# Kernel tuning notes

Measured on AMD Instinct MI355X. Metric: run time of the kernel, lower is better.

## Reference

```python
import jax, jax.numpy as jnp
import numpy as np


def setup_inputs() -> dict:
    key = jax.random.key(0)
    ks = jax.random.split(key, 10)
    B, T, V, D, H = 64, 256, 32000, 512, 1024
    s = lambda fan: 1.0 / np.sqrt(fan)
    return {
        "tokens": jax.random.randint(ks[0], (B, T), 0, V, dtype=jnp.int32),
        "emb": jax.random.normal(ks[1], (V, D), dtype=jnp.float32) * 0.05,
        "W": jax.random.normal(ks[2], (D, 4 * H), dtype=jnp.float32) * s(D),
        "U": jax.random.normal(ks[3], (H, 4 * H), dtype=jnp.float32) * s(H),
        "b": jnp.zeros((4 * H,), dtype=jnp.float32),
        "Wm": jax.random.normal(ks[4], (H, H), dtype=jnp.float32) * s(H),
        "bm": jnp.zeros((H,), dtype=jnp.float32),
        "Wv": jax.random.normal(ks[5], (H, H), dtype=jnp.float32) * s(H),
        "bv": jnp.zeros((H,), dtype=jnp.float32),
        "eps": jax.random.normal(ks[6], (B, H), dtype=jnp.float32),
    }


def _lstm_masked(x_emb, mask, W, U, b):
    # x_emb: [B,T,D], mask: [B,T] bool (True = valid token)
    B, T, D = x_emb.shape
    H = U.shape[0]
    # Precompute input projections for all timesteps: [B,T,4H]
    xW = jnp.einsum('btd,df->btf', x_emb, W) + b

    def step(carry, inp):
        h, c = carry
        xw_t, m_t = inp  # [B,4H], [B]
        z = xw_t + h @ U  # [B,4H]
        i, f, g, o = jnp.split(z, 4, axis=-1)
        i = jax.nn.sigmoid(i)
        f = jax.nn.sigmoid(f)
        g = jnp.tanh(g)
        o = jax.nn.sigmoid(o)
        c_new = f * c + i * g
        h_new = o * jnp.tanh(c_new)
        m = m_t[:, None]
        # Masked timesteps carry state through unchanged (Keras mask_zero semantics)
        h = jnp.where(m, h_new, h)
        c = jnp.where(m, c_new, c)
        return (h, c), None

    h0 = jnp.zeros((B, H), dtype=x_emb.dtype)
    c0 = jnp.zeros((B, H), dtype=x_emb.dtype)
    (h, c), _ = jax.lax.scan(step, (h0, c0),
                             (jnp.swapaxes(xW, 0, 1), jnp.swapaxes(mask, 0, 1)))
    return h


def reference(tokens, emb, W, U, b, Wm, bm, Wv, bv, eps):
    mask = tokens != 0                      # mask_zero=True
    x = emb[tokens]                          # [B,T,D] embedding lookup
    h = _lstm_masked(x, mask, W, U, b)       # [B,H] final state
    mean = h @ Wm + bm
    logvar = h @ Wv + bv
    latent = eps * jnp.exp(logvar * 0.5) + mean   # reparameterization trick
    return latent
```

## Files before the change

kernel.cpp:

```cpp
#include <hip/hip_runtime.h>
#include <stdint.h>

#define BB 64
#define TT 256
#define VV 32000
#define DD 512
#define HH 1024
#define FH 4096

#define UCOL 1040
#define ULDS (128 * UCOL)
#define LSTM_LDS (ULDS + 1024)
#define RSTRIDE (TT * FH * 2)

typedef float f32x4 __attribute__((ext_vector_type(4)));
typedef int   i32x4 __attribute__((ext_vector_type(4)));
typedef __bf16 bf16x8 __attribute__((ext_vector_type(8)));

typedef __attribute__((address_space(1))) void void_g;
typedef __attribute__((address_space(3))) void void_l;

static __device__ __forceinline__ void gload_lds16(const void* g, void* l) {
  __builtin_amdgcn_global_load_lds((const void_g*)g, (void_l*)l, 16, 0, 0);
}

static __device__ __forceinline__ unsigned short f2bf(float f) {
  union { float f; unsigned u; } x; x.f = f;
  unsigned r = x.u + 0x7FFFu + ((x.u >> 16) & 1u);
  return (unsigned short)(r >> 16);
}
static __device__ __forceinline__ float bf2f(unsigned short s) {
  union { unsigned u; float f; } x; x.u = ((unsigned)s) << 16;
  return x.f;
}
static __device__ __forceinline__ i32x4 as_i32x4(uint4 v) {
  union { uint4 u; i32x4 i; } x; x.u = v; return x.i;
}
static __device__ __forceinline__ float sigm(float x) {
  return 1.f / (1.f + __expf(-x));
}
static __device__ __forceinline__ float tanh_f(float x) {
  x = fminf(15.f, fmaxf(-15.f, x));
  float e = __expf(2.f * x);
  return (e - 1.f) / (e + 1.f);
}


__global__ void k_cast_emb(const float* __restrict__ src, unsigned short* __restrict__ dst) {
  size_t i = ((size_t)blockIdx.x * 256 + threadIdx.x) * 8;
  float4 a = *(const float4*)(src + i);
  float4 b = *(const float4*)(src + i + 4);
  uint4 o;
  o.x = (unsigned)f2bf(a.x) | ((unsigned)f2bf(a.y) << 16);
  o.y = (unsigned)f2bf(a.z) | ((unsigned)f2bf(a.w) << 16);
  o.z = (unsigned)f2bf(b.x) | ((unsigned)f2bf(b.y) << 16);
  o.w = (unsigned)f2bf(b.z) | ((unsigned)f2bf(b.w) << 16);
  *(uint4*)(dst + i) = o;
}

__global__ void k_prep_w(const float* __restrict__ Wsrc, unsigned short* __restrict__ Wt) {
  int n = blockIdx.x;
  int k0 = threadIdx.x * 4;
  unsigned short q0 = f2bf(Wsrc[(size_t)(k0 + 0) * FH + n]);
  unsigned short q1 = f2bf(Wsrc[(size_t)(k0 + 1) * FH + n]);
  unsigned short q2 = f2bf(Wsrc[(size_t)(k0 + 2) * FH + n]);
  unsigned short q3 = f2bf(Wsrc[(size_t)(k0 + 3) * FH + n]);
  uint2 o;
  o.x = (unsigned)q0 | ((unsigned)q1 << 16);
  o.y = (unsigned)q2 | ((unsigned)q3 << 16);
  *(uint2*)((char*)Wt + (size_t)n * 1024 + (size_t)k0 * 2) = o;
}

__global__ void k_prep_uq(const float* __restrict__ Usrc, char* __restrict__ Uq,
                          float* __restrict__ su) {
  __shared__ float red[4];
  int bid = blockIdx.x;
  int s = bid >> 7, c = bid & 127;
  int g = c >> 5, m = c & 31;
  int n = g * 1024 + s * 32 + m;
  int tid = threadIdx.x, lane = tid & 63, wid = tid >> 6;
  float v[4];
  float mx = 0.f;
  #pragma unroll
  for (int j = 0; j < 4; ++j) {
    v[j] = Usrc[(size_t)(tid * 4 + j) * FH + n];
    mx = fmaxf(mx, fabsf(v[j]));
  }
  #pragma unroll
  for (int off = 32; off; off >>= 1) mx = fmaxf(mx, __shfl_xor(mx, off));
  if (lane == 0) red[wid] = mx;
  __syncthreads();
  mx = fmaxf(fmaxf(red[0], red[1]), fmaxf(red[2], red[3]));
  float inv = mx > 0.f ? 127.f / mx : 0.f;
  unsigned pk = 0;
  #pragma unroll
  for (int j = 0; j < 4; ++j) {
    int q = __float2int_rn(v[j] * inv);
    pk |= ((unsigned)q & 255u) << (8 * j);
  }
  *(unsigned*)(Uq + (size_t)s * 131072 + (size_t)c * 1024 + tid * 4) = pk;
  if (tid == 0) su[s * 128 + c] = mx / 16129.f;
}

__global__ void k_mask(const int* __restrict__ tok, unsigned long long* __restrict__ mask64) {
  int t = threadIdx.x;
  unsigned long long m = 0;
  for (int b = 0; b < BB; ++b)
    m |= (unsigned long long)(tok[b * TT + t] != 0) << b;
  mask64[t] = m;
}


__launch_bounds__(256)
__global__ void k_gemm_xw(const int* __restrict__ tok, const unsigned short* __restrict__ embb,
                          const unsigned short* __restrict__ Wt, const float* __restrict__ bsrc,
                          unsigned short* __restrict__ xw) {
  __shared__ char As[16384];
  __shared__ char Bs[16384];
  __shared__ int toks[128];
  int tid = threadIdx.x, lane = tid & 63, wid = tid >> 6;
  int bm = blockIdx.x >> 5, bn = blockIdx.x & 31;
  if (tid < 128) toks[tid] = tok[bm * 128 + tid];
  int wm = wid >> 1, wn = wid & 1;
  f32x4 vz = {0.f, 0.f, 0.f, 0.f};
  f32x4 acc[4][4];
  #pragma unroll
  for (int i = 0; i < 4; ++i)
    #pragma unroll
    for (int j = 0; j < 4; ++j) acc[i][j] = vz;

  int kls = (lane >> 4) * 16;
  for (int ks = 0; ks < 8; ++ks) {
    __syncthreads();
    #pragma unroll
    for (int c = 0; c < 4; ++c) {
      int o = wid * 4096 + c * 1024 + lane * 16;
      int m = o >> 7, kl = o & 127;
      const char* ga = (const char*)embb + (size_t)toks[m] * 1024 + ks * 128 + (kl ^ ((m & 7) << 4));
      gload_lds16(ga, As + o);
      const char* gb = (const char*)Wt + (size_t)(bn * 128 + m) * 1024 + ks * 128 + (kl ^ ((m & 7) << 4));
      gload_lds16(gb, Bs + o);
    }
    asm volatile("s_waitcnt vmcnt(0)" ::: "memory");
    __syncthreads();
    #pragma unroll
    for (int tk = 0; tk < 2; ++tk) {
      bf16x8 af[4], bf[4];
      int kb = tk * 64 + kls;
      #pragma unroll
      for (int mt = 0; mt < 4; ++mt) {
        int m = wm * 64 + mt * 16 + (lane & 15);
        af[mt] = *(const bf16x8*)(As + m * 128 + (kb ^ ((m & 7) << 4)));
      }
      #pragma unroll
      for (int nt = 0; nt < 4; ++nt) {
        int n = wn * 64 + nt * 16 + (lane & 15);
        bf[nt] = *(const bf16x8*)(Bs + n * 128 + (kb ^ ((n & 7) << 4)));
      }
      #pragma unroll
      for (int mt = 0; mt < 4; ++mt)
        #pragma unroll
        for (int nt = 0; nt < 4; ++nt)
          acc[mt][nt] = __builtin_amdgcn_mfma_f32_16x16x32_bf16(af[mt], bf[nt], acc[mt][nt], 0, 0, 0);
    }
  }
  #pragma unroll
  for (int nt = 0; nt < 4; ++nt) {
    int n = bn * 128 + wn * 64 + nt * 16 + (lane & 15);
    float bias = bsrc[n];
    int g = n >> 10, hid = n & 1023, s = hid >> 5, m = hid & 31;
    int p = s * 128 + m * 4 + g;
    #pragma unroll
    for (int mt = 0; mt < 4; ++mt) {
      #pragma unroll
      for (int r = 0; r < 4; ++r) {
        int row = bm * 128 + wm * 64 + mt * 16 + (lane >> 4) * 4 + r;
        xw[(size_t)row * FH + p] = f2bf(acc[mt][nt][r] + bias);
      }
    }
  }
}


#define GATE(R) do { \
  unsigned long long x_ = xg[R]; \
  float zi_ = (float)aI[R] * s0 + bf2f((unsigned short)(x_ & 0xFFFFu)); \
  float zf_ = (float)aF[R] * s1 + bf2f((unsigned short)((x_ >> 16) & 0xFFFFu)); \
  float zg_ = (float)aG[R] * s2 + bf2f((unsigned short)((x_ >> 32) & 0xFFFFu)); \
  float zo_ = (float)aO[R] * s3 + bf2f((unsigned short)((x_ >> 48) & 0xFFFFu)); \
  float I_ = sigm(zi_), F_ = sigm(zf_), G_ = tanh_f(zg_), O_ = sigm(zo_); \
  float cn_ = F_ * cst[R] + I_ * G_; \
  float hn_ = O_ * tanh_f(cn_); \
  if (!((mb >> (grp * 16 + lq * 4 + (R))) & 1ull)) { cn_ = cst[R]; hn_ = hst[R]; } \
  cst[R] = cn_; hst[R] = hn_; \
  hs[hh * 320 + (lq * 4 + (R)) * 20 + l15] = (char)__float2int_rn(hn_ * 127.f); \
  if (t == TT - 1) hfin[(size_t)(grp * 16 + lq * 4 + (R)) * 1024 + rank * 32 + hh * 16 + l15] = hn_; \
} while (0)

__launch_bounds__(128, 1)
__global__ void k_lstm(const char* __restrict__ Uq, const float* __restrict__ su,
                       const unsigned short* __restrict__ xw,
                       const unsigned long long* __restrict__ mask64,
                       char* __restrict__ hseq, unsigned* __restrict__ flags,
                       float* __restrict__ hfin) {
  extern __shared__ char smem[];
  char* Us = smem;
  char* hs = smem + ULDS;
  int tid = threadIdx.x, lane = tid & 63, hh = tid >> 6;
  int l15 = lane & 15, lq = lane >> 4;
  int grp = blockIdx.x >> 5, rank = blockIdx.x & 31;
  int m = hh * 16 + l15;

  {
    const char* src = Uq + (size_t)rank * 131072;
    #pragma unroll 4
    for (int i = 0; i < 64; ++i) {
      int o = i * 2048 + tid * 16;
      int c = o >> 10, k = o & 1023;
      *(uint4*)(Us + c * UCOL + k) = *(const uint4*)(src + o);
    }
  }
  __syncthreads();

  float s0 = su[rank * 128 + 0 * 32 + m];
  float s1 = su[rank * 128 + 1 * 32 + m];
  float s2 = su[rank * 128 + 2 * 32 + m];
  float s3 = su[rank * 128 + 3 * 32 + m];
  int bo0 = (0 * 32 + m) * UCOL + lq * 16;
  int bo1 = (1 * 32 + m) * UCOL + lq * 16;
  int bo2 = (2 * 32 + m) * UCOL + lq * 16;
  int bo3 = (3 * 32 + m) * UCOL + lq * 16;

  float cst[4] = {0.f, 0.f, 0.f, 0.f};
  float hst[4] = {0.f, 0.f, 0.f, 0.f};

  const char* xb = (const char*)xw +
      ((size_t)(grp * 16 + lq * 4) * TT * FH + rank * 128 + m * 4) * 2;

  unsigned long long xg[4], xn[4];
  #pragma unroll
  for (int r = 0; r < 4; ++r) xg[r] = *(const unsigned long long*)(xb + (size_t)r * RSTRIDE);

  for (int t = 0; t < TT; ++t) {
    int tn = (t + 1) & 255;
    #pragma unroll
    for (int r = 0; r < 4; ++r)
      xn[r] = *(const unsigned long long*)(xb + (size_t)r * RSTRIDE + (size_t)tn * (FH * 2));
    unsigned long long mb = mask64[t];

    i32x4 aI = {0,0,0,0}, aF = {0,0,0,0}, aG = {0,0,0,0}, aO = {0,0,0,0};

    if (t > 0) {
      const unsigned* fl = flags + (size_t)(t - 1) * 256 + grp * 64;
      for (;;) {
        unsigned v = __hip_atomic_load(fl + lane, __ATOMIC_RELAXED, __HIP_MEMORY_SCOPE_AGENT);
        if (__all(v != 0)) break;
        __builtin_amdgcn_s_sleep(1);
      }
      asm volatile("" ::: "memory");
      const char* hp = hseq + (size_t)(t - 1) * 65536 + (size_t)(grp * 16 + l15) * 1024 + lq * 16;
      uint4 Af[16];
      #pragma unroll
      for (int u = 0; u < 16; ++u) Af[u] = *(const uint4*)(hp + u * 64);
      #pragma unroll
      for (int u = 0; u < 16; ++u) {
        i32x4 a_ = as_i32x4(Af[u]);
        i32x4 b0_ = *(const i32x4*)(Us + bo0 + u * 64);
        i32x4 b1_ = *(const i32x4*)(Us + bo1 + u * 64);
        i32x4 b2_ = *(const i32x4*)(Us + bo2 + u * 64);
        i32x4 b3_ = *(const i32x4*)(Us + bo3 + u * 64);
        aI = __builtin_amdgcn_mfma_i32_16x16x64_i8(a_, b0_, aI, 0, 0, 0);
        aF = __builtin_amdgcn_mfma_i32_16x16x64_i8(a_, b1_, aF, 0, 0, 0);
        aG = __builtin_amdgcn_mfma_i32_16x16x64_i8(a_, b2_, aG, 0, 0, 0);
        aO = __builtin_amdgcn_mfma_i32_16x16x64_i8(a_, b3_, aO, 0, 0, 0);
      }
    }

    GATE(0); GATE(1); GATE(2); GATE(3);

    asm volatile("s_waitcnt lgkmcnt(0)" ::: "memory");
    {
      int prow = lane >> 2, pch = lane & 3;
      unsigned pv = *(const unsigned*)(hs + hh * 320 + prow * 20 + pch * 4);
      __hip_atomic_store(
          (unsigned*)(hseq + (size_t)t * 65536 + (size_t)(grp * 16 + prow) * 1024 +
                      rank * 32 + hh * 16 + pch * 4),
          pv, __ATOMIC_RELAXED, __HIP_MEMORY_SCOPE_AGENT);
    }
    asm volatile("s_waitcnt vmcnt(0)" ::: "memory");
    if (lane == 0)
      __hip_atomic_store(flags + (size_t)t * 256 + grp * 64 + rank * 2 + hh, 1u,
                         __ATOMIC_RELAXED, __HIP_MEMORY_SCOPE_AGENT);

    xg[0] = xn[0]; xg[1] = xn[1]; xg[2] = xn[2]; xg[3] = xn[3];
  }
}


__global__ void k_final(const float* __restrict__ hfin, const float* __restrict__ Wm,
                        const float* __restrict__ bm, const float* __restrict__ Wv,
                        const float* __restrict__ bv, const float* __restrict__ eps,
                        float* __restrict__ out) {
  int jb = blockIdx.x;
  int b = threadIdx.x & 63, u = threadIdx.x >> 6;
  int c0 = jb * 16 + u * 4;
  float am[4] = {0.f, 0.f, 0.f, 0.f};
  float av[4] = {0.f, 0.f, 0.f, 0.f};
  const float* hb = hfin + b * 1024;
  #pragma unroll 2
  for (int k = 0; k < 1024; ++k) {
    float hv = hb[k];
    float4 wm = *(const float4*)(Wm + (size_t)k * 1024 + c0);
    float4 wv = *(const float4*)(Wv + (size_t)k * 1024 + c0);
    am[0] += hv * wm.x; am[1] += hv * wm.y; am[2] += hv * wm.z; am[3] += hv * wm.w;
    av[0] += hv * wv.x; av[1] += hv * wv.y; av[2] += hv * wv.z; av[3] += hv * wv.w;
  }
  #pragma unroll
  for (int i = 0; i < 4; ++i) {
    int c = c0 + i;
    float mean = am[i] + bm[c];
    float lv = av[i] + bv[c];
    out[b * 1024 + c] = eps[b * 1024 + c] * __expf(0.5f * lv) + mean;
  }
}


extern "C" void kernel_launch(void* const* d_in, const int* in_sizes, int n_in,
                              void* d_out, int out_size, void* d_ws, size_t ws_size,
                              hipStream_t stream) {
  const int*   tok = (const int*)d_in[0];
  const float* emb = (const float*)d_in[1];
  const float* W   = (const float*)d_in[2];
  const float* U   = (const float*)d_in[3];
  const float* bia = (const float*)d_in[4];
  const float* Wm  = (const float*)d_in[5];
  const float* bm  = (const float*)d_in[6];
  const float* Wv  = (const float*)d_in[7];
  const float* bv  = (const float*)d_in[8];
  const float* eps = (const float*)d_in[9];
  float* out = (float*)d_out;

  char* ws = (char*)d_ws;
  size_t off = 0;
  auto alloc = [&](size_t sz) { char* p = ws + off; off += (sz + 255) & ~(size_t)255; return p; };
  unsigned short* embb = (unsigned short*)alloc((size_t)VV * DD * 2);
  unsigned short* Wt   = (unsigned short*)alloc((size_t)FH * DD * 2);
  char*  Uq            = (char*)alloc((size_t)32 * 131072);
  float* su            = (float*)alloc((size_t)FH * 4);
  unsigned short* xw   = (unsigned short*)alloc((size_t)BB * TT * FH * 2);
  char*  hseq          = (char*)alloc((size_t)TT * 65536);
  unsigned* flags      = (unsigned*)alloc((size_t)TT * 256 * 4);
  unsigned long long* mask64 = (unsigned long long*)alloc((size_t)TT * 8);
  float* hfin          = (float*)alloc((size_t)BB * HH * 4);
  (void)in_sizes; (void)n_in; (void)out_size; (void)ws_size;

  (void)hipMemsetAsync(flags, 0, (size_t)TT * 256 * 4, stream);
  k_cast_emb<<<8000, 256, 0, stream>>>(emb, embb);
  k_prep_w<<<4096, 128, 0, stream>>>(W, Wt);
  k_prep_uq<<<4096, 256, 0, stream>>>(U, Uq, su);
  k_mask<<<1, 256, 0, stream>>>(tok, mask64);
  k_gemm_xw<<<4096, 256, 0, stream>>>(tok, embb, Wt, bia, xw);
  (void)hipFuncSetAttribute((const void*)k_lstm, hipFuncAttributeMaxDynamicSharedMemorySize, LSTM_LDS);
  k_lstm<<<128, 128, LSTM_LDS, stream>>>(Uq, su, xw, mask64, hseq, flags, hfin);
  k_final<<<64, 256, 0, stream>>>(hfin, Wm, bm, Wv, bv, eps, out);
}
```

Before: 1.884 ms.

## Poll flags per chunk and pipeline h loads with MFMA in LSTM step

Replaces the single all-flags wait before the recurrent matmul with per-chunk polling over 8 groups of producer flags. Each chunk's h-slice load is issued as soon as its producers are ready, and MFMA on earlier chunks overlaps with later waits through triple-buffered registers. Each block starts at a rank-dependent offset to stagger the chunk order. The aim is to overlap cross-block synchronization latency with compute on the serial timestep critical path, at the cost of more polling loops and per-chunk memory fences.

```diff
diff --git a/kernel.cpp b/kernel.cpp
--- a/kernel.cpp
+++ b/kernel.cpp
@@ -197,6 +197,37 @@
   if (t == TT - 1) hfin[(size_t)(grp * 16 + lq * 4 + (R)) * 1024 + rank * 32 + hh * 16 + l15] = hn_; \
 } while (0)
 
+#define POLL8(P) do { \
+  for (;;) { \
+    unsigned v_ = __hip_atomic_load(fl + (P) * 8 + (lane & 7), \
+                                    __ATOMIC_RELAXED, __HIP_MEMORY_SCOPE_AGENT); \
+    if (__all(v_ != 0)) break; \
+    __builtin_amdgcn_s_sleep(1); \
+  } \
+  asm volatile("" ::: "memory"); \
+} while (0)
+
+#define ISSUE(B, P) do { \
+  B[0] = *(const uint4*)(hp + ((P) * 2 + 0) * 64); \
+  B[1] = *(const uint4*)(hp + ((P) * 2 + 1) * 64); \
+} while (0)
+
+#define MFMA2(B, P) do { \
+  _Pragma("unroll") \
+  for (int q_ = 0; q_ < 2; ++q_) { \
+    int u_ = (P) * 2 + q_; \
+    i32x4 a_ = as_i32x4(B[q_]); \
+    i32x4 b0_ = *(const i32x4*)(Us + bo0 + u_ * 64); \
+    i32x4 b1_ = *(const i32x4*)(Us + bo1 + u_ * 64); \
+    i32x4 b2_ = *(const i32x4*)(Us + bo2 + u_ * 64); \
+    i32x4 b3_ = *(const i32x4*)(Us + bo3 + u_ * 64); \
+    aI = __builtin_amdgcn_mfma_i32_16x16x64_i8(a_, b0_, aI, 0, 0, 0); \
+    aF = __builtin_amdgcn_mfma_i32_16x16x64_i8(a_, b1_, aF, 0, 0, 0); \
+    aG = __builtin_amdgcn_mfma_i32_16x16x64_i8(a_, b2_, aG, 0, 0, 0); \
+    aO = __builtin_amdgcn_mfma_i32_16x16x64_i8(a_, b3_, aO, 0, 0, 0); \
+  } \
+} while (0)
+
 __launch_bounds__(128, 1)
 __global__ void k_lstm(const char* __restrict__ Uq, const float* __restrict__ su,
                        const unsigned short* __restrict__ xw,
@@ -237,6 +268,10 @@
   const char* xb = (const char*)xw +
       ((size_t)(grp * 16 + lq * 4) * TT * FH + rank * 128 + m * 4) * 2;
 
+  int p0v = rank >> 2;
+  int P0 = p0v,         P1 = (p0v+1)&7, P2 = (p0v+2)&7, P3 = (p0v+3)&7;
+  int P4 = (p0v+4)&7,   P5 = (p0v+5)&7, P6 = (p0v+6)&7, P7 = (p0v+7)&7;
+
   unsigned long long xg[4], xn[4];
   #pragma unroll
   for (int r = 0; r < 4; ++r) xg[r] = *(const unsigned long long*)(xb + (size_t)r * RSTRIDE);
@@ -252,28 +287,18 @@
 
     if (t > 0) {
       const unsigned* fl = flags + (size_t)(t - 1) * 256 + grp * 64;
-      for (;;) {
-        unsigned v = __hip_atomic_load(fl + lane, __ATOMIC_RELAXED, __HIP_MEMORY_SCOPE_AGENT);
-        if (__all(v != 0)) break;
-        __builtin_amdgcn_s_sleep(1);
-      }
-      asm volatile("" ::: "memory");
       const char* hp = hseq + (size_t)(t - 1) * 65536 + (size_t)(grp * 16 + l15) * 1024 + lq * 16;
-      uint4 Af[16];
-      #pragma unroll
-      for (int u = 0; u < 16; ++u) Af[u] = *(const uint4*)(hp + u * 64);
-      #pragma unroll
-      for (int u = 0; u < 16; ++u) {
-        i32x4 a_ = as_i32x4(Af[u]);
-        i32x4 b0_ = *(const i32x4*)(Us + bo0 + u * 64);
-        i32x4 b1_ = *(const i32x4*)(Us + bo1 + u * 64);
-        i32x4 b2_ = *(const i32x4*)(Us + bo2 + u * 64);
-        i32x4 b3_ = *(const i32x4*)(Us + bo3 + u * 64);
-        aI = __builtin_amdgcn_mfma_i32_16x16x64_i8(a_, b0_, aI, 0, 0, 0);
-        aF = __builtin_amdgcn_mfma_i32_16x16x64_i8(a_, b1_, aF, 0, 0, 0);
-        aG = __builtin_amdgcn_mfma_i32_16x16x64_i8(a_, b2_, aG, 0, 0, 0);
-        aO = __builtin_amdgcn_mfma_i32_16x16x64_i8(a_, b3_, aO, 0, 0, 0);
-      }
+      uint4 B0[2], B1[2], B2[2];
+      POLL8(P0); ISSUE(B0, P0);
+      POLL8(P1); ISSUE(B1, P1);
+      POLL8(P2); ISSUE(B2, P2); MFMA2(B0, P0);
+      POLL8(P3); ISSUE(B0, P3); MFMA2(B1, P1);
+      POLL8(P4); ISSUE(B1, P4); MFMA2(B2, P2);
+      POLL8(P5); ISSUE(B2, P5); MFMA2(B0, P3);
+      POLL8(P6); ISSUE(B0, P6); MFMA2(B1, P4);
+      POLL8(P7); ISSUE(B1, P7); MFMA2(B2, P5);
+      MFMA2(B0, P6);
+      MFMA2(B1, P7);
     }
 
     GATE(0); GATE(1); GATE(2); GATE(3);
```

Result: faster. 1.839 ms (-2.4%).

## Replace per-step flag handshake with sentinel-value polling on the hidden-state buffer

Applied to the files above, without the earlier changes.

Drops the separate flags array in the recurrent LSTM kernel. The hseq buffer is pre-filled with 0x80 bytes, a value int8 quantized h never takes, and consumers poll the hidden-state data itself with cache-bypassing loads until no dword equals the sentinel. The loaded data then feeds the MFMAs directly. This removes the producer's vmcnt wait plus flag store, and the consumer's separate flag-poll round trip, from the critical path of every timestep. In exchange it adds a 16 MB memset, and each retry reloads the full 1 KB per lane. Correctness relies on each dword being written atomically.

```diff
diff --git a/kernel.cpp b/kernel.cpp
--- a/kernel.cpp
+++ b/kernel.cpp
@@ -12,6 +12,7 @@
 #define ULDS (128 * UCOL)
 #define LSTM_LDS (ULDS + 1024)
 #define RSTRIDE (TT * FH * 2)
+#define SENT 0x80808080u
 
 typedef float f32x4 __attribute__((ext_vector_type(4)));
 typedef int   i32x4 __attribute__((ext_vector_type(4)));
@@ -197,12 +198,28 @@
   if (t == TT - 1) hfin[(size_t)(grp * 16 + lq * 4 + (R)) * 1024 + rank * 32 + hh * 16 + l15] = hn_; \
 } while (0)
 
+#define CHK(A) do { \
+  mn = min(mn, (A).x ^ SENT); mn = min(mn, (A).y ^ SENT); \
+  mn = min(mn, (A).z ^ SENT); mn = min(mn, (A).w ^ SENT); \
+} while (0)
+
+#define MFMA1(A, U) do { \
+  i32x4 a_ = as_i32x4(A); \
+  i32x4 b0_ = *(const i32x4*)(Us + bo0 + (U) * 64); \
+  i32x4 b1_ = *(const i32x4*)(Us + bo1 + (U) * 64); \
+  i32x4 b2_ = *(const i32x4*)(Us + bo2 + (U) * 64); \
+  i32x4 b3_ = *(const i32x4*)(Us + bo3 + (U) * 64); \
+  aI = __builtin_amdgcn_mfma_i32_16x16x64_i8(a_, b0_, aI, 0, 0, 0); \
+  aF = __builtin_amdgcn_mfma_i32_16x16x64_i8(a_, b1_, aF, 0, 0, 0); \
+  aG = __builtin_amdgcn_mfma_i32_16x16x64_i8(a_, b2_, aG, 0, 0, 0); \
+  aO = __builtin_amdgcn_mfma_i32_16x16x64_i8(a_, b3_, aO, 0, 0, 0); \
+} while (0)
+
 __launch_bounds__(128, 1)
 __global__ void k_lstm(const char* __restrict__ Uq, const float* __restrict__ su,
                        const unsigned short* __restrict__ xw,
                        const unsigned long long* __restrict__ mask64,
-                       char* __restrict__ hseq, unsigned* __restrict__ flags,
-                       float* __restrict__ hfin) {
+                       char* __restrict__ hseq, float* __restrict__ hfin) {
   extern __shared__ char smem[];
   char* Us = smem;
   char* hs = smem + ULDS;
@@ -237,6 +254,8 @@
   const char* xb = (const char*)xw +
       ((size_t)(grp * 16 + lq * 4) * TT * FH + rank * 128 + m * 4) * 2;
 
+  unsigned voff = (unsigned)(l15 * 1024 + lq * 16);
+
   unsigned long long xg[4], xn[4];
   #pragma unroll
   for (int r = 0; r < 4; ++r) xg[r] = *(const unsigned long long*)(xb + (size_t)r * RSTRIDE);
@@ -251,29 +270,45 @@
     i32x4 aI = {0,0,0,0}, aF = {0,0,0,0}, aG = {0,0,0,0}, aO = {0,0,0,0};
 
     if (t > 0) {
-      const unsigned* fl = flags + (size_t)(t - 1) * 256 + grp * 64;
+      const char* hb = hseq + (size_t)(t - 1) * 65536 + (size_t)grp * 16384;
+      uint4 A0, A1, A2, A3, A4, A5, A6, A7, A8, A9, A10, A11, A12, A13, A14, A15;
       for (;;) {
-        unsigned v = __hip_atomic_load(fl + lane, __ATOMIC_RELAXED, __HIP_MEMORY_SCOPE_AGENT);
-        if (__all(v != 0)) break;
+        asm volatile(
+          "global_load_dwordx4 %0, %16, %17 sc0 sc1\n\t"
+          "global_load_dwordx4 %1, %16, %17 offset:64 sc0 sc1\n\t"
+          "global_load_dwordx4 %2, %16, %17 offset:128 sc0 sc1\n\t"
+          "global_load_dwordx4 %3, %16, %17 offset:192 sc0 sc1\n\t"
+          "global_load_dwordx4 %4, %16, %17 offset:256 sc0 sc1\n\t"
+          "global_load_dwordx4 %5, %16, %17 offset:320 sc0 sc1\n\t"
+          "global_load_dwordx4 %6, %16, %17 offset:384 sc0 sc1\n\t"
+          "global_load_dwordx4 %7, %16, %17 offset:448 sc0 sc1\n\t"
+          "global_load_dwordx4 %8, %16, %17 offset:512 sc0 sc1\n\t"
+          "global_load_dwordx4 %9, %16, %17 offset:576 sc0 sc1\n\t"
+          "global_load_dwordx4 %10, %16, %17 offset:640 sc0 sc1\n\t"
+          "global_load_dwordx4 %11, %16, %17 offset:704 sc0 sc1\n\t"
+          "global_load_dwordx4 %12, %16, %17 offset:768 sc0 sc1\n\t"
+          "global_load_dwordx4 %13, %16, %17 offset:832 sc0 sc1\n\t"
+          "global_load_dwordx4 %14, %16, %17 offset:896 sc0 sc1\n\t"
+          "global_load_dwordx4 %15, %16, %17 offset:960 sc0 sc1\n\t"
+          "s_waitcnt vmcnt(0)"
+          : "=&v"(A0), "=&v"(A1), "=&v"(A2), "=&v"(A3),
+            "=&v"(A4), "=&v"(A5), "=&v"(A6), "=&v"(A7),
+            "=&v"(A8), "=&v"(A9), "=&v"(A10), "=&v"(A11),
+            "=&v"(A12), "=&v"(A13), "=&v"(A14), "=&v"(A15)
+          : "v"(voff), "s"(hb)
+          : "memory");
+        unsigned mn = 0xFFFFFFFFu;
+        CHK(A0);  CHK(A1);  CHK(A2);  CHK(A3);
+        CHK(A4);  CHK(A5);  CHK(A6);  CHK(A7);
+        CHK(A8);  CHK(A9);  CHK(A10); CHK(A11);
+        CHK(A12); CHK(A13); CHK(A14); CHK(A15);
+        if (__all(mn != 0)) break;
         __builtin_amdgcn_s_sleep(1);
       }
-      asm volatile("" ::: "memory");
-      const char* hp = hseq + (size_t)(t - 1) * 65536 + (size_t)(grp * 16 + l15) * 1024 + lq * 16;
-      uint4 Af[16];
-      #pragma unroll
-      for (int u = 0; u < 16; ++u) Af[u] = *(const uint4*)(hp + u * 64);
-      #pragma unroll
-      for (int u = 0; u < 16; ++u) {
-        i32x4 a_ = as_i32x4(Af[u]);
-        i32x4 b0_ = *(const i32x4*)(Us + bo0 + u * 64);
-        i32x4 b1_ = *(const i32x4*)(Us + bo1 + u * 64);
-        i32x4 b2_ = *(const i32x4*)(Us + bo2 + u * 64);
-        i32x4 b3_ = *(const i32x4*)(Us + bo3 + u * 64);
-        aI = __builtin_amdgcn_mfma_i32_16x16x64_i8(a_, b0_, aI, 0, 0, 0);
-        aF = __builtin_amdgcn_mfma_i32_16x16x64_i8(a_, b1_, aF, 0, 0, 0);
-        aG = __builtin_amdgcn_mfma_i32_16x16x64_i8(a_, b2_, aG, 0, 0, 0);
-        aO = __builtin_amdgcn_mfma_i32_16x16x64_i8(a_, b3_, aO, 0, 0, 0);
-      }
+      MFMA1(A0, 0);   MFMA1(A1, 1);   MFMA1(A2, 2);   MFMA1(A3, 3);
+      MFMA1(A4, 4);   MFMA1(A5, 5);   MFMA1(A6, 6);   MFMA1(A7, 7);
+      MFMA1(A8, 8);   MFMA1(A9, 9);   MFMA1(A10, 10); MFMA1(A11, 11);
+      MFMA1(A12, 12); MFMA1(A13, 13); MFMA1(A14, 14); MFMA1(A15, 15);
     }
 
     GATE(0); GATE(1); GATE(2); GATE(3);
@@ -287,10 +322,6 @@
                       rank * 32 + hh * 16 + pch * 4),
           pv, __ATOMIC_RELAXED, __HIP_MEMORY_SCOPE_AGENT);
     }
-    asm volatile("s_waitcnt vmcnt(0)" ::: "memory");
-    if (lane == 0)
-      __hip_atomic_store(flags + (size_t)t * 256 + grp * 64 + rank * 2 + hh, 1u,
-                         __ATOMIC_RELAXED, __HIP_MEMORY_SCOPE_AGENT);
 
     xg[0] = xn[0]; xg[1] = xn[1]; xg[2] = xn[2]; xg[3] = xn[3];
   }
@@ -349,18 +380,17 @@
   float* su            = (float*)alloc((size_t)FH * 4);
   unsigned short* xw   = (unsigned short*)alloc((size_t)BB * TT * FH * 2);
   char*  hseq          = (char*)alloc((size_t)TT * 65536);
-  unsigned* flags      = (unsigned*)alloc((size_t)TT * 256 * 4);
   unsigned long long* mask64 = (unsigned long long*)alloc((size_t)TT * 8);
   float* hfin          = (float*)alloc((size_t)BB * HH * 4);
   (void)in_sizes; (void)n_in; (void)out_size; (void)ws_size;
 
-  (void)hipMemsetAsync(flags, 0, (size_t)TT * 256 * 4, stream);
+  (void)hipMemsetAsync(hseq, 0x80, (size_t)TT * 65536, stream);
   k_cast_emb<<<8000, 256, 0, stream>>>(emb, embb);
   k_prep_w<<<4096, 128, 0, stream>>>(W, Wt);
   k_prep_uq<<<4096, 256, 0, stream>>>(U, Uq, su);
   k_mask<<<1, 256, 0, stream>>>(tok, mask64);
   k_gemm_xw<<<4096, 256, 0, stream>>>(tok, embb, Wt, bia, xw);
   (void)hipFuncSetAttribute((const void*)k_lstm, hipFuncAttributeMaxDynamicSharedMemorySize, LSTM_LDS);
-  k_lstm<<<128, 128, LSTM_LDS, stream>>>(Uq, su, xw, mask64, hseq, flags, hfin);
+  k_lstm<<<128, 128, LSTM_LDS, stream>>>(Uq, su, xw, mask64, hseq, hfin);
   k_final<<<64, 256, 0, stream>>>(hfin, Wm, bm, Wv, bv, eps, out);
 }
```

After: 2.092 ms. +11.0%, slower.
